# Kernel tuning notes

Measured on AMD Instinct MI355X. Metric: run time of the kernel, lower is better.

The kernel has to match this reference:

```python
import jax, jax.numpy as jnp
import numpy as np

# dims
B, S, ENC, MARK = 8, 512, 7, 4
D, I, K, NH = 512, 1024, 4, 8          # embedding_dim, inner=2*D, conv kernel, heads
DH = I // NH                            # 128 per-head dim
BS_BLK = 4                              # qkv_proj_blocksize
NB = I // BS_BLK                        # 256 headwise blocks
L = 4                                   # num_blocks
PRED, COUT = 96, 7
EPS = 1e-6


def ln(x, w):
    mu = jnp.mean(x, -1, keepdims=True)
    var = jnp.var(x, -1, keepdims=True)
    return (x - mu) * jax.lax.rsqrt(var + 1e-5) * w


def causal_conv(x, w, b):
    # x [B,S,I], depthwise causal conv, kernel w [I,K]
    xp = jnp.pad(x, ((0, 0), (K - 1, 0), (0, 0)))
    kern = w.T[:, None, :]  # [K,1,I] for WIO with groups=I
    y = jax.lax.conv_general_dilated(xp, kern, (1,), 'VALID',
                                     dimension_numbers=('NWC', 'WIO', 'NWC'),
                                     feature_group_count=I)
    return y + b


def headwise(t, w):
    # block-diagonal linear (LinearHeadwiseExpand): t [B,S,I], w [NB,BS,BS]
    tb = t.reshape(B, S, NB, BS_BLK)
    return jnp.einsum('bsni,noi->bsno', tb, w).reshape(B, S, I)


def mlstm_parallel(q, k, v, ig, fg):
    # parallel_stabilized_simple: q,k,v [B,NH,S,DH]; ig,fg [B,NH,S]
    lf = jax.nn.log_sigmoid(fg)
    lfc = jnp.concatenate([jnp.zeros_like(lf[..., :1]), jnp.cumsum(lf, -1)], -1)  # [B,NH,S+1]
    m = (lfc[..., :, None] - lfc[..., None, :])[..., 1:, 1:]  # [B,NH,S,S]
    mask = jnp.tril(jnp.ones((S, S), dtype=bool))
    logD = jnp.where(mask, m + ig[..., None, :], -jnp.inf)
    maxD = jnp.max(logD, -1, keepdims=True)
    Dm = jnp.exp(logD - maxD)
    C = jnp.einsum('bnsd,bntd->bnst', q, k) * (DH ** -0.5) * Dm
    n = jnp.maximum(jnp.abs(jnp.sum(C, -1, keepdims=True)), jnp.exp(-maxD))
    return jnp.einsum('bnst,bntd->bnsd', C / (n + EPS), v)


def mh_norm(h, w):
    # per-head layernorm over DH, scale w [I]
    mu = jnp.mean(h, -1, keepdims=True)
    var = jnp.var(h, -1, keepdims=True)
    return (h - mu) * jax.lax.rsqrt(var + 1e-5) * w.reshape(1, NH, 1, DH)


def mlstm_block(x, p):
    lnw, upW, upb, cw, cb, wq, wk, wv, igW, igb, fgW, fgb, onw, skw, dW, db = p
    h = ln(x, lnw)                              # pre-norm
    u = h @ upW + upb                           # [B,S,2I]
    xm, z = jnp.split(u, 2, -1)
    xc = jax.nn.silu(causal_conv(xm, cw, cb))   # conv branch
    q = headwise(xc, wq)
    k = headwise(xc, wk)
    v = headwise(xm, wv)
    g = jnp.concatenate([q, k, v], -1)          # [B,S,3I]
    ig = (g @ igW + igb).transpose(0, 2, 1)     # [B,NH,S]
    fg = (g @ fgW + fgb).transpose(0, 2, 1)
    qh = q.reshape(B, S, NH, DH).transpose(0, 2, 1, 3)
    kh = k.reshape(B, S, NH, DH).transpose(0, 2, 1, 3)
    vh = v.reshape(B, S, NH, DH).transpose(0, 2, 1, 3)
    hh = mlstm_parallel(qh, kh, vh, ig, fg)
    hh = mh_norm(hh, onw).transpose(0, 2, 1, 3).reshape(B, S, I)
    hh = (hh + skw * xc) * jax.nn.silu(z)       # learnable skip + output gate
    return x + hh @ dW + db                     # residual


def setup_inputs() -> dict:
    key = jax.random.key(0)
    ks = jax.random.split(key, 16)
    r = lambda i, shape, s=0.02: jax.random.normal(ks[i], shape, jnp.float32) * s
    return {
        'x_enc': jax.random.normal(ks[0], (B, S, ENC), jnp.float32),
        'x_mark_enc': jax.random.normal(ks[1], (B, S, MARK), jnp.float32),
        'x_dec': jax.random.normal(ks[2], (B, PRED, ENC), jnp.float32),
        'x_mark_dec': jax.random.normal(ks[3], (B, PRED, MARK), jnp.float32),
        'emb_W': r(4, (ENC + MARK, D), 0.1), 'emb_b': jnp.zeros((D,), jnp.float32),
        'blk_ln_w': jnp.ones((L, D), jnp.float32),
        'up_W': r(5, (L, D, 2 * I)), 'up_b': jnp.zeros((L, 2 * I), jnp.float32),
        'conv_w': r(6, (L, I, K), 0.1), 'conv_b': jnp.zeros((L, I), jnp.float32),
        'Wq': r(7, (L, NB, BS_BLK, BS_BLK), 0.3),
        'Wk': r(8, (L, NB, BS_BLK, BS_BLK), 0.3),
        'Wv': r(9, (L, NB, BS_BLK, BS_BLK), 0.3),
        'ig_W': r(10, (L, 3 * I, NH), 0.01), 'ig_b': jnp.full((L, NH), -10.0, jnp.float32),
        'fg_W': r(11, (L, 3 * I, NH), 0.01),
        'fg_b': jnp.tile(jnp.linspace(3.0, 6.0, NH, dtype=jnp.float32)[None], (L, 1)),
        'onorm_w': jnp.ones((L, I), jnp.float32),
        'skip_w': jnp.ones((L, I), jnp.float32),
        'down_W': r(12, (L, I, D)), 'down_b': jnp.zeros((L, D), jnp.float32),
        'post_w': jnp.ones((D,), jnp.float32),
        'head_W': r(13, (D, COUT), 0.05), 'head_b': jnp.zeros((COUT,), jnp.float32),
    }


def reference(x_enc, x_mark_enc, x_dec, x_mark_dec, emb_W, emb_b, blk_ln_w,
              up_W, up_b, conv_w, conv_b, Wq, Wk, Wv, ig_W, ig_b, fg_W, fg_b,
              onorm_w, skip_w, down_W, down_b, post_w, head_W, head_b):
    x = jnp.concatenate([x_enc, x_mark_enc], -1) @ emb_W + emb_b  # [B,S,D]
    params = (blk_ln_w, up_W, up_b, conv_w, conv_b, Wq, Wk, Wv,
              ig_W, ig_b, fg_W, fg_b, onorm_w, skip_w, down_W, down_b)
    def step(c, p):
        return mlstm_block(c, p), None
    x, _ = jax.lax.scan(step, x, params)
    x = ln(x, post_w)                           # post_blocks_norm
    return x[:, -PRED:, :] @ head_W + head_b    # [B,PRED,COUT]
```

## Files before the change

### kernel.cpp

```cpp
#include <hip/hip_runtime.h>
#include <math.h>

static constexpr int kB = 8, kS = 512;
static constexpr int kD = 512, kI = 1024, kNH = 8, kDH = 128;
static constexpr int kL = 4, kPRED = 96, kCOUT = 7;
static constexpr int kM = kB * kS;

typedef __bf16 bf16x8 __attribute__((ext_vector_type(8)));
typedef float f32x4 __attribute__((ext_vector_type(4)));

#define MFMA_BF16(a, b, c) __builtin_amdgcn_mfma_f32_16x16x32_bf16((a), (b), (c), 0, 0, 0)

typedef __attribute__((address_space(1))) const unsigned char* as1cp;
typedef __attribute__((address_space(3))) unsigned char* as3p;
__device__ __forceinline__ void gload16(const void* g, void* l) {
  __builtin_amdgcn_global_load_lds((as1cp)g, (as3p)l, 16, 0, 0);
}

__device__ __forceinline__ unsigned short f2bf(float f) {
  union { float f; unsigned u; } v; v.f = f;
  unsigned r = v.u + 0x7fffu + ((v.u >> 16) & 1u);
  return (unsigned short)(r >> 16);
}
__device__ __forceinline__ float bf2f(unsigned short h) {
  union { unsigned u; float f; } v; v.u = (unsigned)h << 16; return v.f;
}

__global__ __launch_bounds__(256) void embed_ln_kernel(
    const float* __restrict__ xe, const float* __restrict__ xme,
    const float* __restrict__ W, const float* __restrict__ bias,
    const float* __restrict__ lnw,
    float* __restrict__ x, unsigned short* __restrict__ h) {
  int m = blockIdx.x;
  int tid = threadIdx.x;
  __shared__ float f[11];
  if (tid < 7) f[tid] = xe[m * 7 + tid];
  else if (tid < 11) f[tid] = xme[m * 4 + (tid - 7)];
  __syncthreads();
  float v0 = bias[tid], v1 = bias[256 + tid];
#pragma unroll
  for (int e = 0; e < 11; ++e) {
    v0 += f[e] * W[e * kD + tid];
    v1 += f[e] * W[e * kD + 256 + tid];
  }
  x[(size_t)m * kD + tid] = v0;
  x[(size_t)m * kD + 256 + tid] = v1;
  float s1 = v0 + v1, s2 = v0 * v0 + v1 * v1;
#pragma unroll
  for (int o = 1; o < 64; o <<= 1) { s1 += __shfl_xor(s1, o, 64); s2 += __shfl_xor(s2, o, 64); }
  __shared__ float a1[4], a2[4];
  if ((tid & 63) == 0) { a1[tid >> 6] = s1; a2[tid >> 6] = s2; }
  __syncthreads();
  float t1 = a1[0] + a1[1] + a1[2] + a1[3];
  float t2 = a2[0] + a2[1] + a2[2] + a2[3];
  float mu = t1 * (1.f / kD);
  float var = t2 * (1.f / kD) - mu * mu;
  float rs = rsqrtf(var + 1e-5f);
  h[(size_t)m * kD + tid] = f2bf((v0 - mu) * rs * lnw[tid]);
  h[(size_t)m * kD + 256 + tid] = f2bf((v1 - mu) * rs * lnw[256 + tid]);
}

__global__ __launch_bounds__(256) void ln_kernel(
    const float* __restrict__ x, const float* __restrict__ w, unsigned short* __restrict__ h) {
  int m = blockIdx.x, tid = threadIdx.x;
  float v0 = x[(size_t)m * kD + tid];
  float v1 = x[(size_t)m * kD + 256 + tid];
  float s1 = v0 + v1, s2 = v0 * v0 + v1 * v1;
#pragma unroll
  for (int o = 1; o < 64; o <<= 1) { s1 += __shfl_xor(s1, o, 64); s2 += __shfl_xor(s2, o, 64); }
  __shared__ float a1[4], a2[4];
  if ((tid & 63) == 0) { a1[tid >> 6] = s1; a2[tid >> 6] = s2; }
  __syncthreads();
  float t1 = a1[0] + a1[1] + a1[2] + a1[3];
  float t2 = a2[0] + a2[1] + a2[2] + a2[3];
  float mu = t1 * (1.f / kD);
  float var = t2 * (1.f / kD) - mu * mu;
  float rs = rsqrtf(var + 1e-5f);
  h[(size_t)m * kD + tid] = f2bf((v0 - mu) * rs * w[tid]);
  h[(size_t)m * kD + 256 + tid] = f2bf((v1 - mu) * rs * w[256 + tid]);
}

__global__ __launch_bounds__(256) void tpose_w_kernel(
    const float* __restrict__ W, unsigned short* __restrict__ WT, int N, int Kd) {
  int l = blockIdx.z;
  const float* Wl = W + (size_t)l * N * Kd;
  unsigned short* WTl = WT + (size_t)l * N * Kd;
  int n0 = blockIdx.x * 64, k0 = blockIdx.y * 64;
  __shared__ float t[64][65];
  int tid = threadIdx.x;
  for (int idx = tid; idx < 4096; idx += 256) {
    int r = idx >> 6, c = idx & 63;
    t[r][c] = Wl[(size_t)(k0 + r) * N + n0 + c];
  }
  __syncthreads();
  for (int idx = tid; idx < 4096; idx += 256) {
    int r = idx >> 6, c = idx & 63;
    WTl[(size_t)(n0 + r) * Kd + k0 + c] = f2bf(t[c][r]);
  }
}

__global__ __launch_bounds__(256) void tpose_gates_kernel(
    const float* __restrict__ igW, const float* __restrict__ fgW,
    unsigned short* __restrict__ gWT) {
  int l = blockIdx.y;
  int k = blockIdx.x * 256 + threadIdx.x;
  const float* igl = igW + (size_t)l * 3072 * 8;
  const float* fgl = fgW + (size_t)l * 3072 * 8;
  unsigned short* gl = gWT + (size_t)l * 16 * 3072;
#pragma unroll
  for (int h = 0; h < 8; ++h) {
    gl[(size_t)h * 3072 + k] = f2bf(igl[(size_t)k * 8 + h]);
    gl[(size_t)(8 + h) * 3072 + k] = f2bf(fgl[(size_t)k * 8 + h]);
  }
}

template <int BM, int NBN, int RESID, typename TO>
__global__ __launch_bounds__(256) void gemm_mfma_kernel(
    const unsigned short* __restrict__ A, const unsigned short* __restrict__ BT,
    const float* __restrict__ bias, TO* __restrict__ C, int N, int Kd, int nwg) {
  constexpr int A_ISS = BM / 8;
  constexpr int PER_W = (A_ISS + 16) / 4;
  constexpr int MR = BM / 32;
  __shared__ __align__(16) char As[BM * 128];
  __shared__ __align__(16) char Bs[16384];
  int tid = threadIdx.x, w = tid >> 6, l = tid & 63;
  int lr = l & 15, lg = l >> 4;
  int id = blockIdx.x;
  int q = nwg >> 3, r = nwg & 7;
  int xcd = id & 7, pos = id >> 3;
  int wg = (xcd < r ? xcd * (q + 1) : r * (q + 1) + (xcd - r) * q) + pos;
  int bn = wg % NBN, bm = wg / NBN;
  int wrow = (w >> 1) * (BM / 2), wcol = (w & 1) * 64;
  f32x4 acc[MR][4] = {};
  for (int kt = 0; kt < Kd; kt += 64) {
    __syncthreads();
#pragma unroll
    for (int j = 0; j < PER_W; ++j) {
      int g = w * PER_W + j;
      bool isA = g < A_ISS;
      int ii = isA ? g : g - A_ISS;
      int row = ii * 8 + (l >> 3);
      int chunk = (l & 7) ^ (row & 7);
      const unsigned short* src = isA
          ? A + ((size_t)(bm * BM + row) * Kd + kt) + chunk * 8
          : BT + ((size_t)(bn * 128 + row) * Kd + kt) + chunk * 8;
      char* dst = (isA ? As : Bs) + ii * 1024;
      gload16(src, dst);
    }
    __syncthreads();
#pragma unroll
    for (int kk = 0; kk < 2; ++kk) {
      bf16x8 af[MR], bfr[4];
#pragma unroll
      for (int m = 0; m < MR; ++m) {
        int row = wrow + m * 16 + lr;
        int ch = (kk * 4 + lg) ^ (row & 7);
        af[m] = *(const bf16x8*)(As + row * 128 + ch * 16);
      }
#pragma unroll
      for (int n = 0; n < 4; ++n) {
        int row = wcol + n * 16 + lr;
        int ch = (kk * 4 + lg) ^ (row & 7);
        bfr[n] = *(const bf16x8*)(Bs + row * 128 + ch * 16);
      }
      __builtin_amdgcn_s_setprio(1);
#pragma unroll
      for (int m = 0; m < MR; ++m)
#pragma unroll
        for (int n = 0; n < 4; ++n)
          acc[m][n] = MFMA_BF16(af[m], bfr[n], acc[m][n]);
      __builtin_amdgcn_s_setprio(0);
    }
  }
#pragma unroll
  for (int n = 0; n < 4; ++n) {
    int col = bn * 128 + wcol + n * 16 + lr;
    float bv = bias[col];
#pragma unroll
    for (int m = 0; m < MR; ++m)
#pragma unroll
      for (int i = 0; i < 4; ++i) {
        int row = bm * BM + wrow + m * 16 + lg * 4 + i;
        float v = acc[m][n][i] + bv;
        if constexpr (sizeof(TO) == 2) {
          C[(size_t)row * N + col] = (TO)f2bf(v);
        } else {
          if (RESID) v += C[(size_t)row * N + col];
          C[(size_t)row * N + col] = v;
        }
      }
  }
}

__global__ __launch_bounds__(256) void convhead_kernel(
    const unsigned short* __restrict__ u, const float* __restrict__ cw,
    const float* __restrict__ cb,
    const float* __restrict__ Wq, const float* __restrict__ Wk, const float* __restrict__ Wv,
    unsigned short* __restrict__ xcb, unsigned short* __restrict__ qb,
    unsigned short* __restrict__ kb, unsigned short* __restrict__ vb) {
  int m = blockIdx.x;
  int b = m >> 9, s = m & 511;
  int n = threadIdx.x;
  float xm[4][4];
#pragma unroll
  for (int j = 0; j < 4; ++j) {
    int sp = s - 3 + j;
    if (sp >= 0) {
      unsigned long long raw = *(const unsigned long long*)&u[((size_t)(b * kS + sp)) * (2 * kI) + n * 4];
#pragma unroll
      for (int i = 0; i < 4; ++i) xm[j][i] = bf2f((unsigned short)(raw >> (i * 16)));
    } else {
#pragma unroll
      for (int i = 0; i < 4; ++i) xm[j][i] = 0.f;
    }
  }
  float xc[4];
  unsigned long long xcv = 0;
  float4 cb4 = *(const float4*)&cb[n * 4];
  const float* cbp = &cb4.x;
#pragma unroll
  for (int i = 0; i < 4; ++i) {
    int c = n * 4 + i;
    float4 cw4 = *(const float4*)&cw[c * 4];
    float acc = cbp[i] + xm[0][i] * cw4.x + xm[1][i] * cw4.y + xm[2][i] * cw4.z + xm[3][i] * cw4.w;
    xc[i] = acc / (1.f + __expf(-acc));
    xcv |= (unsigned long long)f2bf(xc[i]) << (i * 16);
  }
  *(unsigned long long*)&xcb[(size_t)m * kI + n * 4] = xcv;
  const float* wq = Wq + n * 16;
  const float* wk = Wk + n * 16;
  const float* wv = Wv + n * 16;
  unsigned long long qv = 0, kv = 0, vv = 0;
#pragma unroll
  for (int o = 0; o < 4; ++o) {
    float aq = 0, ak = 0, av = 0;
#pragma unroll
    for (int i = 0; i < 4; ++i) {
      aq += xc[i] * wq[o * 4 + i];
      ak += xc[i] * wk[o * 4 + i];
      av += xm[3][i] * wv[o * 4 + i];
    }
    qv |= (unsigned long long)f2bf(aq) << (o * 16);
    kv |= (unsigned long long)f2bf(ak) << (o * 16);
    vv |= (unsigned long long)f2bf(av) << (o * 16);
  }
  size_t base = ((size_t)(b * 8 + (n >> 5)) * kS + s) * kDH + (n & 31) * 4;
  *(unsigned long long*)&qb[base] = qv;
  *(unsigned long long*)&kb[base] = kv;
  *(unsigned long long*)&vb[base] = vv;
}

__global__ __launch_bounds__(256) void prep_kernel(
    const unsigned short* __restrict__ qb, const unsigned short* __restrict__ kb,
    const unsigned short* __restrict__ vb, const unsigned short* __restrict__ gWT,
    float* __restrict__ IGp, float* __restrict__ FGp, unsigned short* __restrict__ vt) {
  __shared__ __align__(16) char smem[16640];
  int id = blockIdx.x;
  int tid = threadIdx.x;
  if (id < 192) {
    int src = id >> 6;
    int blk = id & 63;
    int b = blk >> 3, s0 = (blk & 7) * 64;
    int w = tid >> 6, l = tid & 63;
    int lr = l & 15, lg = l >> 4;
    char* Ts = smem;
    const unsigned short* srcb = (src == 0) ? qb : (src == 1) ? kb : vb;
    f32x4 acc = {};
    for (int kc8 = 0; kc8 < 8; ++kc8) {
      const unsigned short* srcbase = srcb + ((size_t)(b * 8 + kc8) * kS + s0) * kDH;
      __syncthreads();
#pragma unroll
      for (int j = 0; j < 4; ++j) {
        int issue = w * 4 + j;
        int row = issue * 4 + (l >> 4);
        int chunk = (l & 15) ^ (row & 7);
        gload16(srcbase + row * 128 + chunk * 8, Ts + issue * 1024);
      }
      __syncthreads();
#pragma unroll
      for (int kk = 0; kk < 4; ++kk) {
        int arow = w * 16 + lr;
        int ch = (kk * 4 + lg) ^ (arow & 7);
        bf16x8 af = *(const bf16x8*)(Ts + arow * 256 + ch * 16);
        bf16x8 bfv = *(const bf16x8*)(gWT + (size_t)lr * 3072 + (src * 8 + kc8) * 128 + kk * 32 + lg * 8);
        acc = MFMA_BF16(af, bfv, acc);
      }
    }
    float* IGo = IGp + (size_t)src * 64 * kS;
    float* FGo = FGp + (size_t)src * 64 * kS;
#pragma unroll
    for (int i = 0; i < 4; ++i) {
      int s = s0 + w * 16 + lg * 4 + i;
      if (lr < 8) IGo[((size_t)(b * 8) + lr) * kS + s] = acc[i];
      else FGo[((size_t)(b * 8) + lr - 8) * kS + s] = acc[i];
    }
  } else {
    int t = id - 192;
    int bh = t >> 3, s0 = (t & 7) * 64;
    unsigned short (*tt)[130] = (unsigned short(*)[130])smem;
    for (int idx = tid; idx < 64 * 128; idx += 256) {
      int sl = idx >> 7, d = idx & 127;
      tt[sl][d] = vb[((size_t)bh * kS + s0 + sl) * kDH + d];
    }
    __syncthreads();
    for (int idx = tid; idx < 64 * 128; idx += 256) {
      int dl = idx >> 6, sl = idx & 63;
      vt[((size_t)bh * kDH + dl) * kS + s0 + sl] = tt[sl][dl];
    }
  }
}

__global__ __launch_bounds__(512) void scan_kernel(
    const float* __restrict__ IGp, const float* __restrict__ FGp,
    const float* __restrict__ igb, const float* __restrict__ fgb,
    float* __restrict__ inc, float* __restrict__ a, float* __restrict__ pmax) {
  int bh = blockIdx.x;
  int h = bh & 7;
  int t = threadIdx.x;
  int lane = t & 63, wid = t >> 6;
  const size_t ss = (size_t)64 * kS;
  size_t o = (size_t)bh * kS + t;
  float igv = IGp[o] + IGp[ss + o] + IGp[2 * ss + o] + igb[h];
  float fgv = FGp[o] + FGp[ss + o] + FGp[2 * ss + o] + fgb[h];
  float lf = fminf(fgv, 0.f) - log1pf(__expf(-fabsf(fgv)));
  float x = lf;
#pragma unroll
  for (int off = 1; off < 64; off <<= 1) {
    float v = __shfl_up(x, off, 64);
    if (lane >= off) x += v;
  }
  __shared__ float wsum[8], wmax[8];
  if (lane == 63) wsum[wid] = x;
  __syncthreads();
  float base = 0.f;
  for (int i = 0; i < wid; ++i) base += wsum[i];
  float inct = x + base;
  inc[o] = inct;
  float av = igv - inct;
  a[o] = av;
  float y = av;
#pragma unroll
  for (int off = 1; off < 64; off <<= 1) {
    float v = __shfl_up(y, off, 64);
    if (lane >= off) y = fmaxf(y, v);
  }
  if (lane == 63) wmax[wid] = y;
  __syncthreads();
  float mb = y;
  for (int i = 0; i < wid; ++i) mb = fmaxf(mb, wmax[i]);
  pmax[o] = mb;
}

__global__ __launch_bounds__(512) void mlstm_mfma_kernel(
    const unsigned short* __restrict__ qb, const unsigned short* __restrict__ kb,
    const unsigned short* __restrict__ vt,
    const float* __restrict__ INC, const float* __restrict__ AV, const float* __restrict__ PM,
    const unsigned short* __restrict__ u, const unsigned short* __restrict__ xcb,
    const float* __restrict__ onw, const float* __restrict__ skw,
    unsigned short* __restrict__ hhb) {
  int id = blockIdx.x;
  int bh = (id & 7) * 8 + ((id >> 3) & 7);
  int pr = id >> 6;
  int rtA = 7 - pr, rtB = pr;
  int b = bh >> 3, nh = bh & 7;
  int tid = threadIdx.x, w = tid >> 6, l = tid & 63;
  int g = w >> 2, wl = w & 3;
  int rt = (g == 0) ? rtA : rtB;
  int lr = l & 15, lg = l >> 4;
  __shared__ __align__(16) char Ks[2][16384];
  __shared__ __align__(16) char Vs[2][16384];
  __shared__ __align__(16) char Ps[8][2048];
  __shared__ float avs[512];

  const unsigned short* kbh = kb + (size_t)bh * kS * kDH;
  const unsigned short* vbh = vt + (size_t)bh * kDH * kS;

  avs[tid] = 0.08838834764831845f * __expf(AV[(size_t)bh * kS + tid]);

  bf16x8 qf[4];
  int qrow = rt * 64 + wl * 16 + lr;
  const unsigned short* qrp = qb + ((size_t)bh * kS + qrow) * kDH + lg * 8;
#pragma unroll
  for (int kk = 0; kk < 4; ++kk) qf[kk] = *(const bf16x8*)(qrp + kk * 32);

  float pm_r[4], epm[4];
#pragma unroll
  for (int i = 0; i < 4; ++i) {
    pm_r[i] = PM[(size_t)bh * kS + rt * 64 + wl * 16 + lg * 4 + i];
    epm[i] = __expf(-pm_r[i]);
  }

  f32x4 oacc[8] = {};
  float rsum[4] = {};

#pragma unroll
  for (int j = 0; j < 2; ++j) {
    int issue = w * 2 + j;
    int row = issue * 4 + (l >> 4);
    int chunk = (l & 15) ^ (row & 7);
    gload16(kbh + row * 128 + chunk * 8, Ks[0] + issue * 1024);
  }
#pragma unroll
  for (int j = 0; j < 2; ++j) {
    int vi = w * 2 + j;
    int row = vi * 8 + (l >> 3);
    int chunk = (l & 7) ^ (row & 7);
    gload16(vbh + (size_t)row * kS + chunk * 8, Vs[0] + vi * 1024);
  }
  __syncthreads();

  int cur = 0;
#pragma unroll 1
  for (int ct = 0; ct <= rtA; ++ct) {
    if (ct < rtA) {
      const unsigned short* kbase = kbh + (size_t)(ct + 1) * 64 * kDH;
      const unsigned short* vbase = vbh + (size_t)(ct + 1) * 64;
#pragma unroll
      for (int j = 0; j < 2; ++j) {
        int issue = w * 2 + j;
        int row = issue * 4 + (l >> 4);
        int chunk = (l & 15) ^ (row & 7);
        gload16(kbase + row * 128 + chunk * 8, Ks[cur ^ 1] + issue * 1024);
      }
#pragma unroll
      for (int j = 0; j < 2; ++j) {
        int vi = w * 2 + j;
        int row = vi * 8 + (l >> 3);
        int chunk = (l & 7) ^ (row & 7);
        gload16(vbase + (size_t)row * kS + chunk * 8, Vs[cur ^ 1] + vi * 1024);
      }
    }
    if (ct <= rt) {
      f32x4 sacc[4] = {};
      __builtin_amdgcn_s_setprio(1);
#pragma unroll
      for (int n = 0; n < 4; ++n) {
#pragma unroll
        for (int kk = 0; kk < 4; ++kk) {
          int krow = n * 16 + lr;
          int ch = (kk * 4 + lg) ^ (krow & 7);
          bf16x8 kf = *(const bf16x8*)(Ks[cur] + krow * 256 + ch * 16);
          sacc[n] = MFMA_BF16(qf[kk], kf, sacc[n]);
        }
      }
      __builtin_amdgcn_s_setprio(0);
#pragma unroll
      for (int n = 0; n < 4; ++n) {
        float eav = avs[ct * 64 + n * 16 + lr];
        int cg = ct * 64 + n * 16 + lr;
#pragma unroll
        for (int i = 0; i < 4; ++i) {
          int rg = rt * 64 + wl * 16 + lg * 4 + i;
          float s = 0.f;
          if (ct < rt || cg <= rg)
            s = sacc[n][i] * (eav * epm[i]);
          rsum[i] += s;
          int prow = lg * 4 + i, pcol = n * 16 + lr;
          int byte = prow * 128 + ((((pcol >> 3) ^ (prow & 7))) << 4) + (pcol & 7) * 2;
          *(unsigned short*)(Ps[w] + byte) = f2bf(s);
        }
      }
      __builtin_amdgcn_s_setprio(1);
#pragma unroll
      for (int kk = 0; kk < 2; ++kk) {
        int prow = lr;
        int pch = (kk * 4 + lg) ^ (prow & 7);
        bf16x8 pf = *(const bf16x8*)(Ps[w] + prow * 128 + pch * 16);
#pragma unroll
        for (int nb = 0; nb < 8; ++nb) {
          int vrow = nb * 16 + lr;
          int vch = (kk * 4 + lg) ^ (vrow & 7);
          bf16x8 vf = *(const bf16x8*)(Vs[cur] + vrow * 128 + vch * 16);
          oacc[nb] = MFMA_BF16(pf, vf, oacc[nb]);
        }
      }
      __builtin_amdgcn_s_setprio(0);
    }
    __syncthreads();
    cur ^= 1;
  }

#pragma unroll
  for (int i = 0; i < 4; ++i)
#pragma unroll
    for (int off = 1; off < 16; off <<= 1) rsum[i] += __shfl_xor(rsum[i], off, 16);
  float ninv[4];
#pragma unroll
  for (int i = 0; i < 4; ++i) {
    int rg = rt * 64 + wl * 16 + lg * 4 + i;
    float e0 = __expf(-INC[(size_t)bh * kS + rg] - pm_r[i]);
    float nn = fmaxf(fabsf(rsum[i]), e0);
    ninv[i] = 1.f / (nn + 1e-6f);
  }
  float val[8][4];
  float s1[4] = {}, s2[4] = {};
#pragma unroll
  for (int nb = 0; nb < 8; ++nb)
#pragma unroll
    for (int i = 0; i < 4; ++i) {
      float v = oacc[nb][i] * ninv[i];
      val[nb][i] = v;
      s1[i] += v; s2[i] += v * v;
    }
#pragma unroll
  for (int i = 0; i < 4; ++i) {
#pragma unroll
    for (int off = 1; off < 16; off <<= 1) {
      s1[i] += __shfl_xor(s1[i], off, 16);
      s2[i] += __shfl_xor(s2[i], off, 16);
    }
  }
#pragma unroll
  for (int i = 0; i < 4; ++i) {
    int rg = rt * 64 + wl * 16 + lg * 4 + i;
    float mu = s1[i] * (1.f / 128.f);
    float var = s2[i] * (1.f / 128.f) - mu * mu;
    float rstd = rsqrtf(var + 1e-5f);
    size_t rowbase = (size_t)(b * kS + rg);
#pragma unroll
    for (int nb = 0; nb < 8; ++nb) {
      int c = nh * kDH + nb * 16 + lr;
      float nv = (val[nb][i] - mu) * rstd * onw[c];
      float z = bf2f(u[rowbase * (2 * kI) + kI + c]);
      float sz = z / (1.f + __expf(-z));
      float xcv = bf2f(xcb[rowbase * kI + c]);
      hhb[rowbase * kI + c] = f2bf((nv + skw[c] * xcv) * sz);
    }
  }
}

__global__ __launch_bounds__(256) void head_kernel(
    const float* __restrict__ x, const float* __restrict__ pw,
    const float* __restrict__ hW, const float* __restrict__ hb, float* __restrict__ out) {
  int row = blockIdx.x;
  int b = row / kPRED, p = row % kPRED;
  int m = b * kS + (kS - kPRED) + p;
  int tid = threadIdx.x;
  float v0 = x[(size_t)m * kD + tid];
  float v1 = x[(size_t)m * kD + 256 + tid];
  float s1 = v0 + v1, s2 = v0 * v0 + v1 * v1;
#pragma unroll
  for (int o = 1; o < 64; o <<= 1) { s1 += __shfl_xor(s1, o, 64); s2 += __shfl_xor(s2, o, 64); }
  __shared__ float a1[4], a2[4];
  if ((tid & 63) == 0) { a1[tid >> 6] = s1; a2[tid >> 6] = s2; }
  __syncthreads();
  float t1 = a1[0] + a1[1] + a1[2] + a1[3];
  float t2 = a2[0] + a2[1] + a2[2] + a2[3];
  float mu = t1 * (1.f / kD);
  float var = t2 * (1.f / kD) - mu * mu;
  float rs = rsqrtf(var + 1e-5f);
  __shared__ float buf[512];
  buf[tid] = (v0 - mu) * rs * pw[tid];
  buf[256 + tid] = (v1 - mu) * rs * pw[256 + tid];
  __syncthreads();
  float acc[7] = {};
  for (int kk = tid; kk < 512; kk += 256) {
    float g = buf[kk];
#pragma unroll
    for (int n = 0; n < 7; ++n) acc[n] += g * hW[kk * 7 + n];
  }
  __shared__ float red[256 * 9];
#pragma unroll
  for (int n = 0; n < 7; ++n) red[tid * 9 + n] = acc[n];
  __syncthreads();
  for (int off = 128; off >= 1; off >>= 1) {
    if (tid < off) {
#pragma unroll
      for (int n = 0; n < 7; ++n) red[tid * 9 + n] += red[(tid + off) * 9 + n];
    }
    __syncthreads();
  }
  if (tid < 7) out[(size_t)row * 7 + tid] = red[tid] + hb[tid];
}

extern "C" void kernel_launch(void* const* d_in, const int* in_sizes, int n_in,
                              void* d_out, int out_size, void* d_ws, size_t ws_size,
                              hipStream_t stream) {
  const float* x_enc    = (const float*)d_in[0];
  const float* x_mark   = (const float*)d_in[1];
  const float* emb_W    = (const float*)d_in[4];
  const float* emb_b    = (const float*)d_in[5];
  const float* blk_ln_w = (const float*)d_in[6];
  const float* up_W     = (const float*)d_in[7];
  const float* up_b     = (const float*)d_in[8];
  const float* conv_w   = (const float*)d_in[9];
  const float* conv_b   = (const float*)d_in[10];
  const float* Wq       = (const float*)d_in[11];
  const float* Wk       = (const float*)d_in[12];
  const float* Wv       = (const float*)d_in[13];
  const float* ig_W     = (const float*)d_in[14];
  const float* ig_b     = (const float*)d_in[15];
  const float* fg_W     = (const float*)d_in[16];
  const float* fg_b     = (const float*)d_in[17];
  const float* onorm_w  = (const float*)d_in[18];
  const float* skip_w   = (const float*)d_in[19];
  const float* down_W   = (const float*)d_in[20];
  const float* down_b   = (const float*)d_in[21];
  const float* post_w   = (const float*)d_in[22];
  const float* head_W   = (const float*)d_in[23];
  const float* head_b   = (const float*)d_in[24];
  float* out = (float*)d_out;

  char* ws = (char*)d_ws;
  float* X  = (float*)ws;                     ws += (size_t)kM * kD * 4;
  unsigned short* U    = (unsigned short*)ws; ws += (size_t)kM * 2 * kI * 2;
  unsigned short* XCb  = (unsigned short*)ws; ws += (size_t)kM * kI * 2;
  unsigned short* Hb   = (unsigned short*)ws; ws += (size_t)kM * kD * 2;
  unsigned short* HHb  = (unsigned short*)ws; ws += (size_t)kM * kI * 2;
  unsigned short* qb   = (unsigned short*)ws; ws += (size_t)kM * kI * 2;
  unsigned short* kbuf = (unsigned short*)ws; ws += (size_t)kM * kI * 2;
  unsigned short* vb   = (unsigned short*)ws; ws += (size_t)kM * kI * 2;
  unsigned short* vt   = (unsigned short*)ws; ws += (size_t)kM * kI * 2;
  unsigned short* upWT = (unsigned short*)ws; ws += (size_t)kL * 2 * kI * kD * 2;
  unsigned short* dnWT = (unsigned short*)ws; ws += (size_t)kL * kD * kI * 2;
  unsigned short* gWT  = (unsigned short*)ws; ws += (size_t)kL * 16 * 3072 * 2;
  float* IGp = (float*)ws; ws += (size_t)3 * 64 * kS * 4;
  float* FGp = (float*)ws; ws += (size_t)3 * 64 * kS * 4;
  float* INC = (float*)ws; ws += (size_t)64 * kS * 4;
  float* AV  = (float*)ws; ws += (size_t)64 * kS * 4;
  float* PM  = (float*)ws; ws += (size_t)64 * kS * 4;

  embed_ln_kernel<<<kM, 256, 0, stream>>>(x_enc, x_mark, emb_W, emb_b, blk_ln_w, X, Hb);
  tpose_w_kernel<<<dim3(32, 8, 4), 256, 0, stream>>>(up_W, upWT, 2 * kI, kD);
  tpose_w_kernel<<<dim3(8, 16, 4), 256, 0, stream>>>(down_W, dnWT, kD, kI);
  tpose_gates_kernel<<<dim3(12, 4), 256, 0, stream>>>(ig_W, fg_W, gWT);

  for (int l = 0; l < kL; ++l) {
    const float* lnw  = blk_ln_w + (size_t)l * kD;
    const float* upbl = up_b + (size_t)l * 2 * kI;
    const float* cwl  = conv_w + (size_t)l * kI * 4;
    const float* cbl  = conv_b + (size_t)l * kI;
    const float* wql  = Wq + (size_t)l * 256 * 16;
    const float* wkl  = Wk + (size_t)l * 256 * 16;
    const float* wvl  = Wv + (size_t)l * 256 * 16;
    const float* igbl = ig_b + (size_t)l * kNH;
    const float* fgbl = fg_b + (size_t)l * kNH;
    const float* onwl = onorm_w + (size_t)l * kI;
    const float* skwl = skip_w + (size_t)l * kI;
    const float* dbl  = down_b + (size_t)l * kD;
    const unsigned short* upWTl = upWT + (size_t)l * 2 * kI * kD;
    const unsigned short* dnWTl = dnWT + (size_t)l * kD * kI;
    const unsigned short* gWTl  = gWT + (size_t)l * 16 * 3072;

    if (l > 0) ln_kernel<<<kM, 256, 0, stream>>>(X, lnw, Hb);
    gemm_mfma_kernel<128, 16, 0, unsigned short><<<512, 256, 0, stream>>>(
        Hb, upWTl, upbl, U, 2 * kI, kD, 512);
    convhead_kernel<<<kM, 256, 0, stream>>>(U, cwl, cbl, wql, wkl, wvl, XCb, qb, kbuf, vb);
    prep_kernel<<<704, 256, 0, stream>>>(qb, kbuf, vb, gWTl, IGp, FGp, vt);
    scan_kernel<<<64, 512, 0, stream>>>(IGp, FGp, igbl, fgbl, INC, AV, PM);
    mlstm_mfma_kernel<<<256, 512, 0, stream>>>(
        qb, kbuf, vt, INC, AV, PM, U, XCb, onwl, skwl, HHb);
    gemm_mfma_kernel<64, 4, 1, float><<<256, 256, 0, stream>>>(
        HHb, dnWTl, dbl, X, kD, kI, 256);
  }

  head_kernel<<<kB * kPRED, 256, 0, stream>>>(X, post_w, head_W, head_b, out);
}
```

Before: 444.2 us.

## Fuse gate scan into mLSTM kernel, merge transposes, batch conv rows

Removes the separate scan kernel. Each mLSTM block now recomputes the log-forget-gate cumsum and running max for its head in shared memory while its K/V tiles load, which drops one launch per layer and the INC/AV/PM global round trips. The three weight-transpose launches become one kernel, and convhead now handles four sequence positions per block, reusing the overlapping conv window and the weights kept in registers. The cost is redundant scan work across the row-tile blocks of each head and higher register pressure in convhead.

```diff
diff --git a/kernel.cpp b/kernel.cpp
--- a/kernel.cpp
+++ b/kernel.cpp
@@ -80,37 +80,54 @@
   h[(size_t)m * kD + 256 + tid] = f2bf((v1 - mu) * rs * w[256 + tid]);
 }
 
-__global__ __launch_bounds__(256) void tpose_w_kernel(
-    const float* __restrict__ W, unsigned short* __restrict__ WT, int N, int Kd) {
-  int l = blockIdx.z;
-  const float* Wl = W + (size_t)l * N * Kd;
-  unsigned short* WTl = WT + (size_t)l * N * Kd;
-  int n0 = blockIdx.x * 64, k0 = blockIdx.y * 64;
+__global__ __launch_bounds__(256) void tpose_all_kernel(
+    const float* __restrict__ upW, const float* __restrict__ dnW,
+    const float* __restrict__ igW, const float* __restrict__ fgW,
+    unsigned short* __restrict__ upWT, unsigned short* __restrict__ dnWT,
+    unsigned short* __restrict__ gWT) {
   __shared__ float t[64][65];
-  int tid = threadIdx.x;
-  for (int idx = tid; idx < 4096; idx += 256) {
-    int r = idx >> 6, c = idx & 63;
-    t[r][c] = Wl[(size_t)(k0 + r) * N + n0 + c];
-  }
-  __syncthreads();
-  for (int idx = tid; idx < 4096; idx += 256) {
-    int r = idx >> 6, c = idx & 63;
-    WTl[(size_t)(n0 + r) * Kd + k0 + c] = f2bf(t[c][r]);
-  }
-}
-
-__global__ __launch_bounds__(256) void tpose_gates_kernel(
-    const float* __restrict__ igW, const float* __restrict__ fgW,
-    unsigned short* __restrict__ gWT) {
-  int l = blockIdx.y;
-  int k = blockIdx.x * 256 + threadIdx.x;
-  const float* igl = igW + (size_t)l * 3072 * 8;
-  const float* fgl = fgW + (size_t)l * 3072 * 8;
-  unsigned short* gl = gWT + (size_t)l * 16 * 3072;
-#pragma unroll
-  for (int h = 0; h < 8; ++h) {
-    gl[(size_t)h * 3072 + k] = f2bf(igl[(size_t)k * 8 + h]);
-    gl[(size_t)(8 + h) * 3072 + k] = f2bf(fgl[(size_t)k * 8 + h]);
+  int id = blockIdx.x, tid = threadIdx.x;
+  if (id < 1024) {
+    int l = id >> 8, rem = id & 255;
+    int n0 = (rem >> 3) * 64, k0 = (rem & 7) * 64;
+    const float* Wl = upW + (size_t)l * 2048 * 512;
+    unsigned short* WTl = upWT + (size_t)l * 2048 * 512;
+    for (int idx = tid; idx < 4096; idx += 256) {
+      int r = idx >> 6, c = idx & 63;
+      t[r][c] = Wl[(size_t)(k0 + r) * 2048 + n0 + c];
+    }
+    __syncthreads();
+    for (int idx = tid; idx < 4096; idx += 256) {
+      int r = idx >> 6, c = idx & 63;
+      WTl[(size_t)(n0 + r) * 512 + k0 + c] = f2bf(t[c][r]);
+    }
+  } else if (id < 1536) {
+    int tt = id - 1024;
+    int l = tt >> 7, rem = tt & 127;
+    int n0 = (rem >> 4) * 64, k0 = (rem & 15) * 64;
+    const float* Wl = dnW + (size_t)l * 512 * 1024;
+    unsigned short* WTl = dnWT + (size_t)l * 512 * 1024;
+    for (int idx = tid; idx < 4096; idx += 256) {
+      int r = idx >> 6, c = idx & 63;
+      t[r][c] = Wl[(size_t)(k0 + r) * 512 + n0 + c];
+    }
+    __syncthreads();
+    for (int idx = tid; idx < 4096; idx += 256) {
+      int r = idx >> 6, c = idx & 63;
+      WTl[(size_t)(n0 + r) * 1024 + k0 + c] = f2bf(t[c][r]);
+    }
+  } else {
+    int tt = id - 1536;
+    int l = tt / 12, kc = tt % 12;
+    int k = kc * 256 + tid;
+    const float* igl = igW + (size_t)l * 3072 * 8;
+    const float* fgl = fgW + (size_t)l * 3072 * 8;
+    unsigned short* gl = gWT + (size_t)l * 16 * 3072;
+#pragma unroll
+    for (int h = 0; h < 8; ++h) {
+      gl[(size_t)h * 3072 + k] = f2bf(igl[(size_t)k * 8 + h]);
+      gl[(size_t)(8 + h) * 3072 + k] = f2bf(fgl[(size_t)k * 8 + h]);
+    }
   }
 }
 
@@ -198,13 +215,13 @@
     const float* __restrict__ Wq, const float* __restrict__ Wk, const float* __restrict__ Wv,
     unsigned short* __restrict__ xcb, unsigned short* __restrict__ qb,
     unsigned short* __restrict__ kb, unsigned short* __restrict__ vb) {
-  int m = blockIdx.x;
-  int b = m >> 9, s = m & 511;
+  int mb = blockIdx.x;
+  int b = mb >> 7, sq = (mb & 127) * 4;
   int n = threadIdx.x;
-  float xm[4][4];
-#pragma unroll
-  for (int j = 0; j < 4; ++j) {
-    int sp = s - 3 + j;
+  float xm[7][4];
+#pragma unroll
+  for (int j = 0; j < 7; ++j) {
+    int sp = sq - 3 + j;
     if (sp >= 0) {
       unsigned long long raw = *(const unsigned long long*)&u[((size_t)(b * kS + sp)) * (2 * kI) + n * 4];
 #pragma unroll
@@ -214,40 +231,50 @@
       for (int i = 0; i < 4; ++i) xm[j][i] = 0.f;
     }
   }
-  float xc[4];
-  unsigned long long xcv = 0;
   float4 cb4 = *(const float4*)&cb[n * 4];
   const float* cbp = &cb4.x;
-#pragma unroll
-  for (int i = 0; i < 4; ++i) {
-    int c = n * 4 + i;
-    float4 cw4 = *(const float4*)&cw[c * 4];
-    float acc = cbp[i] + xm[0][i] * cw4.x + xm[1][i] * cw4.y + xm[2][i] * cw4.z + xm[3][i] * cw4.w;
-    xc[i] = acc / (1.f + __expf(-acc));
-    xcv |= (unsigned long long)f2bf(xc[i]) << (i * 16);
-  }
-  *(unsigned long long*)&xcb[(size_t)m * kI + n * 4] = xcv;
-  const float* wq = Wq + n * 16;
-  const float* wk = Wk + n * 16;
-  const float* wv = Wv + n * 16;
-  unsigned long long qv = 0, kv = 0, vv = 0;
-#pragma unroll
-  for (int o = 0; o < 4; ++o) {
-    float aq = 0, ak = 0, av = 0;
+  float cwv[4][4];
+#pragma unroll
+  for (int i = 0; i < 4; ++i) *(float4*)cwv[i] = *(const float4*)&cw[(n * 4 + i) * 4];
+  float wqv[16], wkv[16], wvv[16];
+#pragma unroll
+  for (int o2 = 0; o2 < 4; ++o2) {
+    *(float4*)&wqv[o2 * 4] = *(const float4*)&Wq[n * 16 + o2 * 4];
+    *(float4*)&wkv[o2 * 4] = *(const float4*)&Wk[n * 16 + o2 * 4];
+    *(float4*)&wvv[o2 * 4] = *(const float4*)&Wv[n * 16 + o2 * 4];
+  }
+#pragma unroll
+  for (int t = 0; t < 4; ++t) {
+    int s = sq + t;
+    float xc[4];
+    unsigned long long xcv = 0;
 #pragma unroll
     for (int i = 0; i < 4; ++i) {
-      aq += xc[i] * wq[o * 4 + i];
-      ak += xc[i] * wk[o * 4 + i];
-      av += xm[3][i] * wv[o * 4 + i];
-    }
-    qv |= (unsigned long long)f2bf(aq) << (o * 16);
-    kv |= (unsigned long long)f2bf(ak) << (o * 16);
-    vv |= (unsigned long long)f2bf(av) << (o * 16);
-  }
-  size_t base = ((size_t)(b * 8 + (n >> 5)) * kS + s) * kDH + (n & 31) * 4;
-  *(unsigned long long*)&qb[base] = qv;
-  *(unsigned long long*)&kb[base] = kv;
-  *(unsigned long long*)&vb[base] = vv;
+      float acc = cbp[i] + xm[t][i] * cwv[i][0] + xm[t + 1][i] * cwv[i][1] +
+                  xm[t + 2][i] * cwv[i][2] + xm[t + 3][i] * cwv[i][3];
+      xc[i] = acc / (1.f + __expf(-acc));
+      xcv |= (unsigned long long)f2bf(xc[i]) << (i * 16);
+    }
+    *(unsigned long long*)&xcb[((size_t)(b * kS + s)) * kI + n * 4] = xcv;
+    unsigned long long qv = 0, kv = 0, vv = 0;
+#pragma unroll
+    for (int o = 0; o < 4; ++o) {
+      float aq = 0, ak = 0, av = 0;
+#pragma unroll
+      for (int i = 0; i < 4; ++i) {
+        aq += xc[i] * wqv[o * 4 + i];
+        ak += xc[i] * wkv[o * 4 + i];
+        av += xm[t + 3][i] * wvv[o * 4 + i];
+      }
+      qv |= (unsigned long long)f2bf(aq) << (o * 16);
+      kv |= (unsigned long long)f2bf(ak) << (o * 16);
+      vv |= (unsigned long long)f2bf(av) << (o * 16);
+    }
+    size_t base = ((size_t)(b * 8 + (n >> 5)) * kS + s) * kDH + (n & 31) * 4;
+    *(unsigned long long*)&qb[base] = qv;
+    *(unsigned long long*)&kb[base] = kv;
+    *(unsigned long long*)&vb[base] = vv;
+  }
 }
 
 __global__ __launch_bounds__(256) void prep_kernel(
@@ -310,51 +337,11 @@
   }
 }
 
-__global__ __launch_bounds__(512) void scan_kernel(
-    const float* __restrict__ IGp, const float* __restrict__ FGp,
-    const float* __restrict__ igb, const float* __restrict__ fgb,
-    float* __restrict__ inc, float* __restrict__ a, float* __restrict__ pmax) {
-  int bh = blockIdx.x;
-  int h = bh & 7;
-  int t = threadIdx.x;
-  int lane = t & 63, wid = t >> 6;
-  const size_t ss = (size_t)64 * kS;
-  size_t o = (size_t)bh * kS + t;
-  float igv = IGp[o] + IGp[ss + o] + IGp[2 * ss + o] + igb[h];
-  float fgv = FGp[o] + FGp[ss + o] + FGp[2 * ss + o] + fgb[h];
-  float lf = fminf(fgv, 0.f) - log1pf(__expf(-fabsf(fgv)));
-  float x = lf;
-#pragma unroll
-  for (int off = 1; off < 64; off <<= 1) {
-    float v = __shfl_up(x, off, 64);
-    if (lane >= off) x += v;
-  }
-  __shared__ float wsum[8], wmax[8];
-  if (lane == 63) wsum[wid] = x;
-  __syncthreads();
-  float base = 0.f;
-  for (int i = 0; i < wid; ++i) base += wsum[i];
-  float inct = x + base;
-  inc[o] = inct;
-  float av = igv - inct;
-  a[o] = av;
-  float y = av;
-#pragma unroll
-  for (int off = 1; off < 64; off <<= 1) {
-    float v = __shfl_up(y, off, 64);
-    if (lane >= off) y = fmaxf(y, v);
-  }
-  if (lane == 63) wmax[wid] = y;
-  __syncthreads();
-  float mb = y;
-  for (int i = 0; i < wid; ++i) mb = fmaxf(mb, wmax[i]);
-  pmax[o] = mb;
-}
-
 __global__ __launch_bounds__(512) void mlstm_mfma_kernel(
     const unsigned short* __restrict__ qb, const unsigned short* __restrict__ kb,
     const unsigned short* __restrict__ vt,
-    const float* __restrict__ INC, const float* __restrict__ AV, const float* __restrict__ PM,
+    const float* __restrict__ IGp, const float* __restrict__ FGp,
+    const float* __restrict__ igb, const float* __restrict__ fgb,
     const unsigned short* __restrict__ u, const unsigned short* __restrict__ xcb,
     const float* __restrict__ onw, const float* __restrict__ skw,
     unsigned short* __restrict__ hhb) {
@@ -370,28 +357,11 @@
   __shared__ __align__(16) char Ks[2][16384];
   __shared__ __align__(16) char Vs[2][16384];
   __shared__ __align__(16) char Ps[8][2048];
-  __shared__ float avs[512];
+  __shared__ float avs[512], incs[512], pms[512];
+  __shared__ float wsum[8], wmax[8];
 
   const unsigned short* kbh = kb + (size_t)bh * kS * kDH;
   const unsigned short* vbh = vt + (size_t)bh * kDH * kS;
-
-  avs[tid] = 0.08838834764831845f * __expf(AV[(size_t)bh * kS + tid]);
-
-  bf16x8 qf[4];
-  int qrow = rt * 64 + wl * 16 + lr;
-  const unsigned short* qrp = qb + ((size_t)bh * kS + qrow) * kDH + lg * 8;
-#pragma unroll
-  for (int kk = 0; kk < 4; ++kk) qf[kk] = *(const bf16x8*)(qrp + kk * 32);
-
-  float pm_r[4], epm[4];
-#pragma unroll
-  for (int i = 0; i < 4; ++i) {
-    pm_r[i] = PM[(size_t)bh * kS + rt * 64 + wl * 16 + lg * 4 + i];
-    epm[i] = __expf(-pm_r[i]);
-  }
-
-  f32x4 oacc[8] = {};
-  float rsum[4] = {};
 
 #pragma unroll
   for (int j = 0; j < 2; ++j) {
@@ -407,7 +377,58 @@
     int chunk = (l & 7) ^ (row & 7);
     gload16(vbh + (size_t)row * kS + chunk * 8, Vs[0] + vi * 1024);
   }
+
+  {
+    int lane = tid & 63, wid2 = tid >> 6;
+    const size_t ss = (size_t)64 * kS;
+    size_t o = (size_t)bh * kS + tid;
+    float igv = IGp[o] + IGp[ss + o] + IGp[2 * ss + o] + igb[nh];
+    float fgv = FGp[o] + FGp[ss + o] + FGp[2 * ss + o] + fgb[nh];
+    float lf = fminf(fgv, 0.f) - log1pf(__expf(-fabsf(fgv)));
+    float x = lf;
+#pragma unroll
+    for (int off = 1; off < 64; off <<= 1) {
+      float v = __shfl_up(x, off, 64);
+      if (lane >= off) x += v;
+    }
+    if (lane == 63) wsum[wid2] = x;
+    __syncthreads();
+    float base = 0.f;
+    for (int i2 = 0; i2 < wid2; ++i2) base += wsum[i2];
+    float inct = x + base;
+    incs[tid] = inct;
+    float av = igv - inct;
+    avs[tid] = 0.08838834764831845f * __expf(av);
+    float y = av;
+#pragma unroll
+    for (int off = 1; off < 64; off <<= 1) {
+      float v = __shfl_up(y, off, 64);
+      if (lane >= off) y = fmaxf(y, v);
+    }
+    if (lane == 63) wmax[wid2] = y;
+    __syncthreads();
+    float mb2 = y;
+    for (int i2 = 0; i2 < wid2; ++i2) mb2 = fmaxf(mb2, wmax[i2]);
+    pms[tid] = mb2;
+  }
+
+  bf16x8 qf[4];
+  int qrow = rt * 64 + wl * 16 + lr;
+  const unsigned short* qrp = qb + ((size_t)bh * kS + qrow) * kDH + lg * 8;
+#pragma unroll
+  for (int kk = 0; kk < 4; ++kk) qf[kk] = *(const bf16x8*)(qrp + kk * 32);
+
   __syncthreads();
+
+  float pm_r[4], epm[4];
+#pragma unroll
+  for (int i = 0; i < 4; ++i) {
+    pm_r[i] = pms[rt * 64 + wl * 16 + lg * 4 + i];
+    epm[i] = __expf(-pm_r[i]);
+  }
+
+  f32x4 oacc[8] = {};
+  float rsum[4] = {};
 
   int cur = 0;
 #pragma unroll 1
@@ -488,7 +509,7 @@
 #pragma unroll
   for (int i = 0; i < 4; ++i) {
     int rg = rt * 64 + wl * 16 + lg * 4 + i;
-    float e0 = __expf(-INC[(size_t)bh * kS + rg] - pm_r[i]);
+    float e0 = __expf(-incs[rg] - pm_r[i]);
     float nn = fmaxf(fabsf(rsum[i]), e0);
     ninv[i] = 1.f / (nn + 1e-6f);
   }
@@ -616,14 +637,9 @@
   unsigned short* gWT  = (unsigned short*)ws; ws += (size_t)kL * 16 * 3072 * 2;
   float* IGp = (float*)ws; ws += (size_t)3 * 64 * kS * 4;
   float* FGp = (float*)ws; ws += (size_t)3 * 64 * kS * 4;
-  float* INC = (float*)ws; ws += (size_t)64 * kS * 4;
-  float* AV  = (float*)ws; ws += (size_t)64 * kS * 4;
-  float* PM  = (float*)ws; ws += (size_t)64 * kS * 4;
 
   embed_ln_kernel<<<kM, 256, 0, stream>>>(x_enc, x_mark, emb_W, emb_b, blk_ln_w, X, Hb);
-  tpose_w_kernel<<<dim3(32, 8, 4), 256, 0, stream>>>(up_W, upWT, 2 * kI, kD);
-  tpose_w_kernel<<<dim3(8, 16, 4), 256, 0, stream>>>(down_W, dnWT, kD, kI);
-  tpose_gates_kernel<<<dim3(12, 4), 256, 0, stream>>>(ig_W, fg_W, gWT);
+  tpose_all_kernel<<<1584, 256, 0, stream>>>(up_W, down_W, ig_W, fg_W, upWT, dnWT, gWT);
 
   for (int l = 0; l < kL; ++l) {
     const float* lnw  = blk_ln_w + (size_t)l * kD;
@@ -645,11 +661,10 @@
     if (l > 0) ln_kernel<<<kM, 256, 0, stream>>>(X, lnw, Hb);
     gemm_mfma_kernel<128, 16, 0, unsigned short><<<512, 256, 0, stream>>>(
         Hb, upWTl, upbl, U, 2 * kI, kD, 512);
-    convhead_kernel<<<kM, 256, 0, stream>>>(U, cwl, cbl, wql, wkl, wvl, XCb, qb, kbuf, vb);
+    convhead_kernel<<<1024, 256, 0, stream>>>(U, cwl, cbl, wql, wkl, wvl, XCb, qb, kbuf, vb);
     prep_kernel<<<704, 256, 0, stream>>>(qb, kbuf, vb, gWTl, IGp, FGp, vt);
-    scan_kernel<<<64, 512, 0, stream>>>(IGp, FGp, igbl, fgbl, INC, AV, PM);
     mlstm_mfma_kernel<<<256, 512, 0, stream>>>(
-        qb, kbuf, vt, INC, AV, PM, U, XCb, onwl, skwl, HHb);
+        qb, kbuf, vt, IGp, FGp, igbl, fgbl, U, XCb, onwl, skwl, HHb);
     gemm_mfma_kernel<64, 4, 1, float><<<256, 256, 0, stream>>>(
         HHb, dnWTl, dbl, X, kD, kI, 256);
   }
```

New measurement: 388.4 us. 12.6% less time.
